# Kernel optimization log

Hardware: AMD Instinct MI355X
Metric: run time of the kernel (lower is better)

The kernel has to match this reference:

```python
import jax, jax.numpy as jnp
import numpy as np

LOSS_WEIGHT = 1.0
STRIDE = 4.0
KEY_W = 0.5
BETA = 1.0 / STRIDE
BOUND2 = 1000.0 ** 2
TIME = 10


def _smooth_l1(pred, target):
    diff = jnp.abs(pred - target)
    return jnp.where(diff < BETA, 0.5 * diff * diff / BETA, diff - 0.5 * BETA)


def _interpolate(poly):
    # poly: (N, P, 2) -> (N, P*TIME, 2), linear interp between each pt and its roll-by-1 neighbor
    N, P, _ = poly.shape
    roll = jnp.roll(poly, shift=1, axis=1)
    step = jnp.arange(TIME, dtype=poly.dtype) / TIME          # (TIME,)
    interp = poly[:, :, None, :] * step[None, None, :, None] \
           + roll[:, :, None, :] * (1.0 - step)[None, None, :, None]  # (N,P,TIME,2)
    return interp.reshape(N, P * TIME, 2)


def _pairwise_sqdist(a, b):
    # matches compute_distance(pred_poly=a, gt_poly=b): out[n, j, i] = ||a[n,i] - b[n,j]||^2
    return jnp.sum((a[:, None, :, :] - b[:, :, None, :]) ** 2, axis=-1)  # (N, Mb, Ma)


def _masked_mean(loss, mask):
    # mean over selected (K, 2) elements, i.e. sum / (count*2)
    cnt = jnp.sum(mask.astype(loss.dtype)) * 2.0
    return jnp.sum(loss * mask[..., None].astype(loss.dtype)) / jnp.maximum(cnt, 1.0)


def setup_inputs() -> dict:
    key = jax.random.key(0)
    k1, k2, k3, k4, k5 = jax.random.split(key, 5)
    N, P = 256, 128
    return {
        "pred_contours": jax.random.normal(k1, (N, P, 2), jnp.float32),
        "pred_offsets": jax.random.normal(k2, (N, P, 2), jnp.float32),
        "gt_contours": jax.random.normal(k3, (N, P, 2), jnp.float32),
        "gt_key_points": jax.random.normal(k4, (N, P, 2), jnp.float32),
        "gt_key_points_mask": jax.random.randint(k5, (N, P), 0, 2, jnp.int32),
    }


def reference(pred_contours, pred_offsets, gt_contours, gt_key_points, gt_key_points_mask):
    masks = gt_key_points_mask.astype(bool)

    # ---- item 1: each pred point matched to nearest interpolated gt point ----
    targets = _interpolate(gt_contours)                       # (N, P*TIME, 2)
    d1 = _pairwise_sqdist(pred_contours, targets)             # (N, P*TIME, P)
    matched1 = jnp.min(d1, axis=1)                            # (N, P)
    idx_gt = jnp.argmin(d1, axis=1)                           # (N, P)
    valid1 = matched1 <= BOUND2
    tgt = jnp.take_along_axis(targets, idx_gt[..., None], axis=1)  # (N, P, 2)
    off_t1 = jax.lax.stop_gradient((tgt - pred_contours) / STRIDE)
    loss1 = _masked_mean(_smooth_l1(pred_offsets, off_t1), valid1) * (1.0 - KEY_W)

    # ---- item 2: each gt key point matched to nearest pred point ----
    d2 = _pairwise_sqdist(gt_key_points, pred_contours)       # (N, Ppred, Pkey)
    matched2 = jnp.min(d2, axis=1)                            # (N, Pkey)
    idx_pred = jnp.argmin(d2, axis=1)                         # (N, Pkey)
    valid2 = (matched2 <= BOUND2) & masks
    preds_g = jnp.take_along_axis(pred_contours, idx_pred[..., None], axis=1)
    offs_g = jnp.take_along_axis(pred_offsets, idx_pred[..., None], axis=1)
    off_t2 = jax.lax.stop_gradient((gt_key_points - preds_g) / STRIDE)
    loss2 = _masked_mean(_smooth_l1(offs_g, off_t2), valid2) * KEY_W

    return (loss1 + loss2) * LOSS_WEIGHT
```

## Files before the change

kernel.cpp:

```cpp
#include <hip/hip_runtime.h>


constexpr int N_ = 256;
constexpr int P_ = 128;

__device__ __forceinline__ float smooth_l1(float diff) {
  float a = fabsf(diff);
  return (a < 0.25f) ? (2.0f * a * a) : (a - 0.125f);
}

__global__ __launch_bounds__(1024) void dm_partial_kernel(
    const float* __restrict__ pred_c, const float* __restrict__ pred_o,
    const float* __restrict__ gt_c,  const float* __restrict__ gt_k,
    const int* __restrict__ mask, float4* __restrict__ partial)
{
  const int n   = blockIdx.x;
  const int tid = threadIdx.x;
  const int i   = tid & (P_ - 1);
  const int q   = tid >> 7;

  __shared__ float2 pc[P_];
  __shared__ float2 po[P_];
  __shared__ float4 segA[P_];
  __shared__ float2 segE[P_];
  __shared__ float  segI[P_];
  __shared__ float  st[12];
  __shared__ float  bd[8][P_];
  __shared__ int    bj[8][P_];
  __shared__ float4 redw[16];

  const float2* pc_g = (const float2*)pred_c + n * P_;
  const float2* po_g = (const float2*)pred_o + n * P_;
  const float2* gc_g = (const float2*)gt_c  + n * P_;
  const float2* gk_g = (const float2*)gt_k  + n * P_;

  if (tid < P_) {
    int p = tid;
    float2 a = gc_g[p];
    float2 b = gc_g[(p + P_ - 1) & (P_ - 1)];
    segA[p] = make_float4(a.x, a.y, b.x, b.y);
    float ex = a.x - b.x, ey = a.y - b.y;
    segE[p] = make_float2(ex, ey);
    float e2 = ex * ex + ey * ey;
    segI[p] = (e2 > 0.0f) ? (1.0f / e2) : 0.0f;
  } else if (tid < 2 * P_) {
    pc[tid - P_] = pc_g[tid - P_];
  } else if (tid < 3 * P_) {
    po[tid - 2 * P_] = po_g[tid - 2 * P_];
  } else if (tid < 3 * P_ + 10) {
    int t = tid - 3 * P_;
    st[t] = (float)t / 10.0f;
  }
  __syncthreads();

  const float2 pt = pc[i];
  float best = 3.0e38f; int bestj = 0;
  {
    const int p0 = q * 16;
    #pragma unroll 4
    for (int p = p0; p < p0 + 16; ++p) {
      float4 ab  = segA[p];
      float2 e   = segE[p];
      float  inv = segI[p];
      float fx = ab.z - pt.x, fy = ab.w - pt.y;
      float ef = e.x * fx + e.y * fy;
      float tf = -(ef * inv) * 10.0f;
      int tl = (int)floorf(tf);
      tl = min(max(tl, 0), 8);
      float s0 = st[tl], s1v = st[tl + 1];
      float ns0 = 1.0f - s0, ns1 = 1.0f - s1v;
      float v0x = ab.x * s0 + ab.z * ns0;
      float v0y = ab.y * s0 + ab.w * ns0;
      float v1x = ab.x * s1v + ab.z * ns1;
      float v1y = ab.y * s1v + ab.w * ns1;
      float dx0 = pt.x - v0x, dy0 = pt.y - v0y;
      float dx1 = pt.x - v1x, dy1 = pt.y - v1y;
      float d0 = dx0 * dx0 + dy0 * dy0;
      float d1 = dx1 * dx1 + dy1 * dy1;
      bool c  = d1 < d0;
      float dl = c ? d1 : d0;
      int   jl = p * 10 + (c ? tl + 1 : tl);
      if (dl < best) { best = dl; bestj = jl; }
    }
  }
  bd[q][i] = best; bj[q][i] = bestj;
  __syncthreads();

  float s1 = 0.0f, c1 = 0.0f;
  if (q == 0) {
    float bb = bd[0][i]; int jj = bj[0][i];
    #pragma unroll
    for (int w = 1; w < 8; ++w) {
      float d = bd[w][i];
      if (d < bb) { bb = d; jj = bj[w][i]; }
    }
    if (bb <= 1.0e6f) {
      int p = jj / 10, t = jj - (jj / 10) * 10;
      float4 ab = segA[p];
      float s  = st[t], ns = 1.0f - s;
      float vx = ab.x * s + ab.z * ns;
      float vy = ab.y * s + ab.w * ns;
      float2 o = po[i];
      float tx = (vx - pt.x) * 0.25f;
      float ty = (vy - pt.y) * 0.25f;
      s1 = smooth_l1(o.x - tx) + smooth_l1(o.y - ty);
      c1 = 1.0f;
    }
  }
  __syncthreads();

  const float2 k = gk_g[i];
  float best2 = 3.0e38f; int bestj2 = 0;
  {
    const int j0 = q * 16;
    #pragma unroll 4
    for (int j = j0; j < j0 + 16; ++j) {
      float2 pp = pc[j];
      float dx = k.x - pp.x, dy = k.y - pp.y;
      float d = dx * dx + dy * dy;
      if (d < best2) { best2 = d; bestj2 = j; }
    }
  }
  bd[q][i] = best2; bj[q][i] = bestj2;
  __syncthreads();

  float s2 = 0.0f, c2 = 0.0f;
  if (q == 0) {
    float bb = bd[0][i]; int jj = bj[0][i];
    #pragma unroll
    for (int w = 1; w < 8; ++w) {
      float d = bd[w][i];
      if (d < bb) { bb = d; jj = bj[w][i]; }
    }
    if (bb <= 1.0e6f && mask[n * P_ + i] != 0) {
      float2 pp = pc[jj];
      float2 o  = po[jj];
      float tx = (k.x - pp.x) * 0.25f;
      float ty = (k.y - pp.y) * 0.25f;
      s2 = smooth_l1(o.x - tx) + smooth_l1(o.y - ty);
      c2 = 1.0f;
    }
  }

  #pragma unroll
  for (int off = 32; off > 0; off >>= 1) {
    s1 += __shfl_down(s1, off);
    c1 += __shfl_down(c1, off);
    s2 += __shfl_down(s2, off);
    c2 += __shfl_down(c2, off);
  }
  const int wave = tid >> 6;
  const int lane = tid & 63;
  if (lane == 0) redw[wave] = make_float4(s1, c1, s2, c2);
  __syncthreads();
  if (tid == 0) {
    float4 r = redw[0];
    #pragma unroll
    for (int w = 1; w < 16; ++w) {
      float4 v = redw[w];
      r.x += v.x; r.y += v.y; r.z += v.z; r.w += v.w;
    }
    partial[n] = r;
  }
}

__global__ __launch_bounds__(256) void dm_final_kernel(
    const float4* __restrict__ partial, float* __restrict__ out)
{
  const int tid = threadIdx.x;
  float4 v = partial[tid];
  float s1 = v.x, c1 = v.y, s2 = v.z, c2 = v.w;
  #pragma unroll
  for (int off = 32; off > 0; off >>= 1) {
    s1 += __shfl_down(s1, off);
    c1 += __shfl_down(c1, off);
    s2 += __shfl_down(s2, off);
    c2 += __shfl_down(c2, off);
  }
  __shared__ float4 redv[4];
  const int wave = tid >> 6;
  const int lane = tid & 63;
  if (lane == 0) redv[wave] = make_float4(s1, c1, s2, c2);
  __syncthreads();
  if (tid == 0) {
    float4 r = redv[0];
    #pragma unroll
    for (int w = 1; w < 4; ++w) {
      float4 q = redv[w];
      r.x += q.x; r.y += q.y; r.z += q.z; r.w += q.w;
    }
    float l1 = (r.x / fmaxf(r.y * 2.0f, 1.0f)) * 0.5f;
    float l2 = (r.z / fmaxf(r.w * 2.0f, 1.0f)) * 0.5f;
    out[0] = l1 + l2;
  }
}

extern "C" void kernel_launch(void* const* d_in, const int* in_sizes, int n_in,
                              void* d_out, int out_size, void* d_ws, size_t ws_size,
                              hipStream_t stream) {
  const float* pred_c = (const float*)d_in[0];
  const float* pred_o = (const float*)d_in[1];
  const float* gt_c   = (const float*)d_in[2];
  const float* gt_k   = (const float*)d_in[3];
  const int*   mask   = (const int*)d_in[4];
  float4* partial = (float4*)d_ws;

  dm_partial_kernel<<<N_, 1024, 0, stream>>>(pred_c, pred_o, gt_c, gt_k, mask, partial);
  dm_final_kernel<<<1, 256, 0, stream>>>(partial, (float*)d_out);
}
```

Measured before the change: 69.20 us.

## Fuse final reduction via cooperative grid sync and merge both matching phases

Replaces the two-kernel launch with one cooperative kernel that does a grid-wide sync and lets block 0 run the final reduction. Both nearest-neighbour searches now run back to back before a single barrier, using separate shared buffers. The two per-point finalisations run on different waves (q==0 and q==1) so they proceed in parallel. This removes a kernel launch and two block barriers, in exchange for grid-sync overhead, more shared memory, and requiring all 256 blocks of 1024 threads to be co-resident.

```diff
diff --git a/kernel.cpp b/kernel.cpp
--- a/kernel.cpp
+++ b/kernel.cpp
@@ -1,4 +1,7 @@
 #include <hip/hip_runtime.h>
+#include <hip/hip_cooperative_groups.h>
+
+namespace cg = cooperative_groups;
 
 
 constexpr int N_ = 256;
@@ -9,10 +12,11 @@
   return (a < 0.25f) ? (2.0f * a * a) : (a - 0.125f);
 }
 
-__global__ __launch_bounds__(1024) void dm_partial_kernel(
+__global__ __launch_bounds__(1024) void dm_fused_kernel(
     const float* __restrict__ pred_c, const float* __restrict__ pred_o,
     const float* __restrict__ gt_c,  const float* __restrict__ gt_k,
-    const int* __restrict__ mask, float4* __restrict__ partial)
+    const int* __restrict__ mask, float4* __restrict__ partial,
+    float* __restrict__ out)
 {
   const int n   = blockIdx.x;
   const int tid = threadIdx.x;
@@ -25,14 +29,19 @@
   __shared__ float2 segE[P_];
   __shared__ float  segI[P_];
   __shared__ float  st[12];
-  __shared__ float  bd[8][P_];
-  __shared__ int    bj[8][P_];
+  __shared__ float  bd1[8][P_];
+  __shared__ int    bj1[8][P_];
+  __shared__ float  bd2[8][P_];
+  __shared__ int    bj2[8][P_];
   __shared__ float4 redw[16];
 
   const float2* pc_g = (const float2*)pred_c + n * P_;
   const float2* po_g = (const float2*)pred_o + n * P_;
   const float2* gc_g = (const float2*)gt_c  + n * P_;
   const float2* gk_g = (const float2*)gt_k  + n * P_;
+
+  const float2 kpt = gk_g[i];
+  const int    mk  = (q == 1) ? mask[n * P_ + i] : 0;
 
   if (tid < P_) {
     int p = tid;
@@ -54,8 +63,8 @@
   __syncthreads();
 
   const float2 pt = pc[i];
-  float best = 3.0e38f; int bestj = 0;
   {
+    float best = 3.0e38f; int bestj = 0;
     const int p0 = q * 16;
     #pragma unroll 4
     for (int p = p0; p < p0 + 16; ++p) {
@@ -82,17 +91,30 @@
       int   jl = p * 10 + (c ? tl + 1 : tl);
       if (dl < best) { best = dl; bestj = jl; }
     }
-  }
-  bd[q][i] = best; bj[q][i] = bestj;
+    bd1[q][i] = best; bj1[q][i] = bestj;
+  }
+
+  {
+    float best2 = 3.0e38f; int bestj2 = 0;
+    const int j0 = q * 16;
+    #pragma unroll 4
+    for (int j = j0; j < j0 + 16; ++j) {
+      float2 pp = pc[j];
+      float dx = kpt.x - pp.x, dy = kpt.y - pp.y;
+      float d = dx * dx + dy * dy;
+      if (d < best2) { best2 = d; bestj2 = j; }
+    }
+    bd2[q][i] = best2; bj2[q][i] = bestj2;
+  }
   __syncthreads();
 
-  float s1 = 0.0f, c1 = 0.0f;
+  float s1 = 0.0f, c1 = 0.0f, s2 = 0.0f, c2 = 0.0f;
   if (q == 0) {
-    float bb = bd[0][i]; int jj = bj[0][i];
+    float bb = bd1[0][i]; int jj = bj1[0][i];
     #pragma unroll
     for (int w = 1; w < 8; ++w) {
-      float d = bd[w][i];
-      if (d < bb) { bb = d; jj = bj[w][i]; }
+      float d = bd1[w][i];
+      if (d < bb) { bb = d; jj = bj1[w][i]; }
     }
     if (bb <= 1.0e6f) {
       int p = jj / 10, t = jj - (jj / 10) * 10;
@@ -106,37 +128,18 @@
       s1 = smooth_l1(o.x - tx) + smooth_l1(o.y - ty);
       c1 = 1.0f;
     }
-  }
-  __syncthreads();
-
-  const float2 k = gk_g[i];
-  float best2 = 3.0e38f; int bestj2 = 0;
-  {
-    const int j0 = q * 16;
-    #pragma unroll 4
-    for (int j = j0; j < j0 + 16; ++j) {
-      float2 pp = pc[j];
-      float dx = k.x - pp.x, dy = k.y - pp.y;
-      float d = dx * dx + dy * dy;
-      if (d < best2) { best2 = d; bestj2 = j; }
-    }
-  }
-  bd[q][i] = best2; bj[q][i] = bestj2;
-  __syncthreads();
-
-  float s2 = 0.0f, c2 = 0.0f;
-  if (q == 0) {
-    float bb = bd[0][i]; int jj = bj[0][i];
+  } else if (q == 1) {
+    float bb = bd2[0][i]; int jj = bj2[0][i];
     #pragma unroll
     for (int w = 1; w < 8; ++w) {
-      float d = bd[w][i];
-      if (d < bb) { bb = d; jj = bj[w][i]; }
-    }
-    if (bb <= 1.0e6f && mask[n * P_ + i] != 0) {
+      float d = bd2[w][i];
+      if (d < bb) { bb = d; jj = bj2[w][i]; }
+    }
+    if (bb <= 1.0e6f && mk != 0) {
       float2 pp = pc[jj];
       float2 o  = po[jj];
-      float tx = (k.x - pp.x) * 0.25f;
-      float ty = (k.y - pp.y) * 0.25f;
+      float tx = (kpt.x - pp.x) * 0.25f;
+      float ty = (kpt.y - pp.y) * 0.25f;
       s2 = smooth_l1(o.x - tx) + smooth_l1(o.y - ty);
       c2 = 1.0f;
     }
@@ -161,37 +164,38 @@
       r.x += v.x; r.y += v.y; r.z += v.z; r.w += v.w;
     }
     partial[n] = r;
-  }
-}
-
-__global__ __launch_bounds__(256) void dm_final_kernel(
-    const float4* __restrict__ partial, float* __restrict__ out)
-{
-  const int tid = threadIdx.x;
-  float4 v = partial[tid];
-  float s1 = v.x, c1 = v.y, s2 = v.z, c2 = v.w;
-  #pragma unroll
-  for (int off = 32; off > 0; off >>= 1) {
-    s1 += __shfl_down(s1, off);
-    c1 += __shfl_down(c1, off);
-    s2 += __shfl_down(s2, off);
-    c2 += __shfl_down(c2, off);
-  }
-  __shared__ float4 redv[4];
-  const int wave = tid >> 6;
-  const int lane = tid & 63;
-  if (lane == 0) redv[wave] = make_float4(s1, c1, s2, c2);
-  __syncthreads();
-  if (tid == 0) {
-    float4 r = redv[0];
-    #pragma unroll
-    for (int w = 1; w < 4; ++w) {
-      float4 q = redv[w];
-      r.x += q.x; r.y += q.y; r.z += q.z; r.w += q.w;
-    }
-    float l1 = (r.x / fmaxf(r.y * 2.0f, 1.0f)) * 0.5f;
-    float l2 = (r.z / fmaxf(r.w * 2.0f, 1.0f)) * 0.5f;
-    out[0] = l1 + l2;
+    __threadfence();
+  }
+
+  cg::this_grid().sync();
+
+  if (n == 0) {
+    __threadfence();
+    float a = 0.0f, b = 0.0f, c = 0.0f, d = 0.0f;
+    if (tid < N_) {
+      float4 v = partial[tid];
+      a = v.x; b = v.y; c = v.z; d = v.w;
+    }
+    #pragma unroll
+    for (int off = 32; off > 0; off >>= 1) {
+      a += __shfl_down(a, off);
+      b += __shfl_down(b, off);
+      c += __shfl_down(c, off);
+      d += __shfl_down(d, off);
+    }
+    if (lane == 0) redw[wave] = make_float4(a, b, c, d);
+    __syncthreads();
+    if (tid == 0) {
+      float4 r = redw[0];
+      #pragma unroll
+      for (int w = 1; w < 16; ++w) {
+        float4 v = redw[w];
+        r.x += v.x; r.y += v.y; r.z += v.z; r.w += v.w;
+      }
+      float l1 = (r.x / fmaxf(r.y * 2.0f, 1.0f)) * 0.5f;
+      float l2 = (r.z / fmaxf(r.w * 2.0f, 1.0f)) * 0.5f;
+      out[0] = l1 + l2;
+    }
   }
 }
 
@@ -202,9 +206,12 @@
   const float* pred_o = (const float*)d_in[1];
   const float* gt_c   = (const float*)d_in[2];
   const float* gt_k   = (const float*)d_in[3];
-  const int*   mask   = (const int*)d_in[4];
+  const int*   maskp  = (const int*)d_in[4];
   float4* partial = (float4*)d_ws;
-
-  dm_partial_kernel<<<N_, 1024, 0, stream>>>(pred_c, pred_o, gt_c, gt_k, mask, partial);
-  dm_final_kernel<<<1, 256, 0, stream>>>(partial, (float*)d_out);
+  float*  outp    = (float*)d_out;
+
+  void* args[] = {(void*)&pred_c, (void*)&pred_o, (void*)&gt_c, (void*)&gt_k,
+                  (void*)&maskp, (void*)&partial, (void*)&outp};
+  hipLaunchCooperativeKernel(dm_fused_kernel, dim3(N_), dim3(1024),
+                             args, 0, stream);
 }
```

Measured after the change: 120.2 us. +73.7%, slower.
